# Optimization experiments

Measured on AMD Instinct MI355X. Metric: run time of the kernel, lower is better.

Reference implementation:

```python
import jax, jax.numpy as jnp
import numpy as np

NUM_HEADS = 16
WINDOW = 128
PERSIST = 16


def setup_inputs() -> dict:
    key = jax.random.key(0)
    ks = jax.random.split(key, 6)
    B, S, D, L = 2, 2048, 2048, 512
    sd = 1.0 / np.sqrt(D)
    sl = 1.0 / np.sqrt(L)
    return {
        "x": jax.random.normal(ks[0], (B, S, D), dtype=jnp.float32),
        "Wq": jax.random.normal(ks[1], (D, D), dtype=jnp.float32) * sd,
        "Wkv": jax.random.normal(ks[2], (D, L), dtype=jnp.float32) * sd,
        "Wk": jax.random.normal(ks[3], (L, D), dtype=jnp.float32) * sl,
        "Wv": jax.random.normal(ks[4], (L, D), dtype=jnp.float32) * sl,
        "Wo": jax.random.normal(ks[5], (D, D), dtype=jnp.float32) * sd,
    }


def reference(x, Wq, Wkv, Wk, Wv, Wo):
    B, S, D = x.shape
    H = NUM_HEADS
    hd = D // H
    scale = hd ** -0.5

    q = (x @ Wq).reshape(B, S, H, hd)
    kv_latent = x @ Wkv                      # MLA-style latent bottleneck
    k = (kv_latent @ Wk).reshape(B, S, H, hd)
    v = (kv_latent @ Wv).reshape(B, S, H, hd)

    # causal + sliding-window + persistent attention-sink mask
    qi = jnp.arange(S)[:, None]
    ki = jnp.arange(S)[None, :]
    mask = (ki <= qi) & ((qi - ki < WINDOW) | (ki < PERSIST))  # [S,S]

    scores = jnp.einsum("bqhd,bkhd->bhqk", q, k) * scale
    scores = jnp.where(mask[None, None], scores, jnp.finfo(scores.dtype).min)
    attn = jax.nn.softmax(scores, axis=-1)
    out = jnp.einsum("bhqk,bkhd->bqhd", attn, v).reshape(B, S, D)
    return out @ Wo
```

## Files before the change

kernel.cpp:

```cpp
#include <hip/hip_runtime.h>

typedef float f32x4 __attribute__((ext_vector_type(4)));
typedef float f32x16 __attribute__((ext_vector_type(16)));
typedef __bf16 bf16x8 __attribute__((ext_vector_type(8)));

__device__ __forceinline__ short f2bf(float f) {
    union { float f; unsigned u; } x; x.f = f;
    unsigned r = x.u + 0x7fffu + ((x.u >> 16) & 1u);
    return (short)(r >> 16);
}

__device__ __forceinline__ void store_out(float* p, float v) { *p = v; }
__device__ __forceinline__ void store_out(short* p, float v) { *p = f2bf(v); }

__device__ __forceinline__ void gload_lds16(const short* g, short* l) {
    __builtin_amdgcn_global_load_lds(
        (__attribute__((address_space(1))) void*)(void*)g,
        (__attribute__((address_space(3))) void*)l, 16, 0, 0);
}

__global__ void prep_all(const float* __restrict__ x, short* __restrict__ xb,
                         const float* __restrict__ Wq, const float* __restrict__ Wkv,
                         short* __restrict__ WqkvT) {
    __shared__ float tile[32][33];
    int id = blockIdx.x;
    const int t = threadIdx.x;
    if (id < 8192) {
        const int i = id * 256 + t;
        float4 v = ((const float4*)x)[i];
        ((short4*)xb)[i] = make_short4(f2bf(v.x), f2bf(v.y), f2bf(v.z), f2bf(v.w));
        return;
    }
    id -= 8192;
    const float* in; short* out; int R, C, xt, yt;
    if (id < 4096) { in = Wq;  out = WqkvT; R = 2048; C = 2048; xt = id & 63; yt = id >> 6; }
    else           { id -= 4096; in = Wkv; out = WqkvT + (size_t)2048 * 2048;
                     R = 2048; C = 512; xt = id & 15; yt = id >> 4; }
    const int c0 = xt * 32, r0 = yt * 32;
    const int tx = t & 31, ty = t >> 5;
#pragma unroll
    for (int i = 0; i < 32; i += 8)
        tile[ty + i][tx] = in[(size_t)(r0 + ty + i) * C + c0 + tx];
    __syncthreads();
#pragma unroll
    for (int i = 0; i < 32; i += 8)
        out[(size_t)(c0 + ty + i) * R + r0 + tx] = f2bf(tile[tx][ty + i]);
}

template <typename OutT>
__device__ __forceinline__ void gemm32_core(
    const short* __restrict__ A, const short* __restrict__ Bt, OutT* __restrict__ C,
    int m0, int n0, int K, int lda, int ldb, int ldc, short* sA, short* sB) {
    const int t = threadIdx.x;
    const int w = t >> 6, l = t & 63;
    const int wr = w >> 1, wc = w & 1;
    const int lrow = l & 31, lhalf = l >> 5;

    f32x16 acc[2][2] = {};

    const int r_off = w * 32 + (l >> 3);
    const int c8 = (((l & 7) ^ (l >> 3)) & 7) * 8;
    const short* aB = A + (size_t)(m0 + r_off) * lda + c8;
    const short* bB = Bt + (size_t)(n0 + r_off) * ldb + c8;
    short* sAw = sA + w * 2048;
    short* sBw = sB + w * 2048;

    for (int kk = 0; kk < K; kk += 64) {
#pragma unroll
        for (int p = 0; p < 4; ++p) {
            gload_lds16(aB + kk + (size_t)(p * 8) * lda, sAw + p * 512);
            gload_lds16(bB + kk + (size_t)(p * 8) * ldb, sBw + p * 512);
        }
        __syncthreads();
#pragma unroll
        for (int ks = 0; ks < 4; ++ks) {
            const int c = ks * 2 + lhalf;
            bf16x8 af[2], bfr[2];
#pragma unroll
            for (int mi = 0; mi < 2; ++mi) {
                const int m = wr * 64 + mi * 32 + lrow;
                af[mi] = *(const bf16x8*)&sA[m * 64 + (c ^ (m & 7)) * 8];
            }
#pragma unroll
            for (int ni = 0; ni < 2; ++ni) {
                const int n = wc * 64 + ni * 32 + lrow;
                bfr[ni] = *(const bf16x8*)&sB[n * 64 + (c ^ (n & 7)) * 8];
            }
#pragma unroll
            for (int mi = 0; mi < 2; ++mi)
#pragma unroll
                for (int ni = 0; ni < 2; ++ni)
                    acc[mi][ni] = __builtin_amdgcn_mfma_f32_32x32x16_bf16(
                        af[mi], bfr[ni], acc[mi][ni], 0, 0, 0);
        }
        __syncthreads();
    }
#pragma unroll
    for (int mi = 0; mi < 2; ++mi)
#pragma unroll
        for (int ni = 0; ni < 2; ++ni) {
            const int col = n0 + wc * 64 + ni * 32 + lrow;
#pragma unroll
            for (int r = 0; r < 16; ++r) {
                const int row = m0 + wr * 64 + mi * 32 + (r & 3) + 8 * (r >> 2) + 4 * lhalf;
                store_out(&C[(size_t)row * ldc + col], acc[mi][ni][r]);
            }
        }
}

__global__ __launch_bounds__(256, 2)
void gemm32qkv(const short* __restrict__ A, const short* __restrict__ Bt,
               short* __restrict__ C,
               const float* __restrict__ Wo, const float* __restrict__ Wk,
               const float* __restrict__ Wv,
               short* __restrict__ WoT, short* __restrict__ WkT,
               short* __restrict__ WvT) {
    __shared__ __align__(16) short sA[128 * 64];
    __shared__ __align__(16) short sB[128 * 64];
    int id = blockIdx.x;
    if (id < 640) {
        gemm32_core<short>(A, Bt, C, (id / 20) * 128, (id % 20) * 128,
                           2048, 2048, 2048, 2560, sA, sB);
        return;
    }
    id -= 640;
    float (*tile)[33] = (float(*)[33])sA;
    const float* in; short* out; int R, Cc, xt, yt;
    if (id < 4096)      { in = Wo; out = WoT; R = 2048; Cc = 2048; xt = id & 63; yt = id >> 6; }
    else if (id < 5120) { id -= 4096; in = Wk; out = WkT; R = 512; Cc = 2048; xt = id & 63; yt = id >> 6; }
    else                { id -= 5120; in = Wv; out = WvT; R = 512; Cc = 2048; xt = id & 63; yt = id >> 6; }
    const int c0 = xt * 32, r0 = yt * 32;
    const int t = threadIdx.x;
    const int tx = t & 31, ty = t >> 5;
#pragma unroll
    for (int i = 0; i < 32; i += 8)
        tile[ty + i][tx] = in[(size_t)(r0 + ty + i) * Cc + c0 + tx];
    __syncthreads();
#pragma unroll
    for (int i = 0; i < 32; i += 8)
        out[(size_t)(c0 + ty + i) * R + r0 + tx] = f2bf(tile[tx][ty + i]);
}

#define LBASE(buf, kh, ab) ((((((buf) << 1) | (kh)) << 1) | (ab)) * 8192)

#define STAGE(P, ld, tt, kh, buf, ab)                                   \
    do {                                                                \
        const int kb_ = (tt) * 64 + (kh) * 32;                          \
        const short* s_ = (P) + kb_;                                    \
        short* d_ = lds + LBASE(buf, kh, ab) + w * 512;                 \
        gload_lds16(s_, d_);                                            \
        gload_lds16(s_ + (size_t)128 * (ld), d_ + 4096);                \
    } while (0)

#define VM6 asm volatile("s_waitcnt vmcnt(6)" ::: "memory")

#define MFMA16(a, b, c) __builtin_amdgcn_mfma_f32_16x16x32_bf16(a, b, c, 0, 0, 0)

#define MM_ROW(mi, areg)                                                \
    acc[mi][0] = MFMA16(areg, bv0, acc[mi][0]);                         \
    acc[mi][1] = MFMA16(areg, bv1, acc[mi][1]);                         \
    acc[mi][2] = MFMA16(areg, bv2, acc[mi][2]);                         \
    acc[mi][3] = MFMA16(areg, bv3, acc[mi][3]);

#define HALFK(buf, kh, STG0, W0, STG1)                                  \
    {                                                                   \
        bf16x8 bv0, bv1, bv2, bv3;                                      \
        {                                                               \
            const short* Ab_ = lds + LBASE(buf, kh, 0) + (wm * 128) * 32 + foff; \
            const short* Bb_ = lds + LBASE(buf, kh, 1) + (wn * 64) * 32 + foff;  \
            bf16x8 a0_ = *(const bf16x8*)&Ab_[0];                       \
            bf16x8 a1_ = *(const bf16x8*)&Ab_[512];                     \
            bf16x8 a2_ = *(const bf16x8*)&Ab_[1024];                    \
            bf16x8 a3_ = *(const bf16x8*)&Ab_[1536];                    \
            bv0 = *(const bf16x8*)&Bb_[0];                              \
            bv1 = *(const bf16x8*)&Bb_[512];                            \
            bv2 = *(const bf16x8*)&Bb_[1024];                           \
            bv3 = *(const bf16x8*)&Bb_[1536];                           \
            STG0;                                                       \
            W0;                                                         \
            __builtin_amdgcn_s_barrier();                               \
            asm volatile("s_waitcnt lgkmcnt(0)" ::: "memory");          \
            __builtin_amdgcn_sched_barrier(0);                          \
            __builtin_amdgcn_s_setprio(1);                              \
            MM_ROW(0, a0_) MM_ROW(1, a1_) MM_ROW(2, a2_) MM_ROW(3, a3_) \
            __builtin_amdgcn_s_setprio(0);                              \
            __builtin_amdgcn_s_barrier();                               \
        }                                                               \
        {                                                               \
            const short* Ab_ = lds + LBASE(buf, kh, 0) + (wm * 128 + 64) * 32 + foff; \
            bf16x8 a0_ = *(const bf16x8*)&Ab_[0];                       \
            bf16x8 a1_ = *(const bf16x8*)&Ab_[512];                     \
            bf16x8 a2_ = *(const bf16x8*)&Ab_[1024];                    \
            bf16x8 a3_ = *(const bf16x8*)&Ab_[1536];                    \
            STG1;                                                       \
            __builtin_amdgcn_s_barrier();                               \
            asm volatile("s_waitcnt lgkmcnt(0)" ::: "memory");          \
            __builtin_amdgcn_sched_barrier(0);                          \
            __builtin_amdgcn_s_setprio(1);                              \
            MM_ROW(4, a0_) MM_ROW(5, a1_) MM_ROW(6, a2_) MM_ROW(7, a3_) \
            __builtin_amdgcn_s_setprio(0);                              \
            __builtin_amdgcn_s_barrier();                               \
        }                                                               \
    }

template <typename OutT>
__device__ __forceinline__ void gemm256_core(
    const short* __restrict__ A, const short* __restrict__ Bt, OutT* __restrict__ C,
    int m0, int n0, int K, int lda, int ldb, int ldc, short* lds) {
    const int t = threadIdx.x;
    const int w = t >> 6, l = t & 63;
    const int wm = w >> 2, wn = w & 3;
    const int l15 = l & 15, lc = l >> 4;

    const int su = (l & 7) ^ ((l >> 3) & 7);
    const int srow = (w << 4) + ((l >> 3) << 1) + (su >> 2);
    const int scol = (su & 3) << 3;
    const short* Ag = A + (size_t)(m0 + srow) * lda + scol;
    const short* Bg = Bt + (size_t)(n0 + srow) * ldb + scol;

    const int i3 = ((((l15 & 1) << 2) | lc) ^ ((l15 >> 1) & 7));
    const int foff = (l15 >> 1) * 64 + i3 * 8;

    f32x4 acc[8][4] = {};

    const int ntm1 = (K >> 6) - 1;
    const int niter = K >> 7;

    STAGE(Ag, lda, 0, 0, 0, 0);
    STAGE(Bg, ldb, 0, 0, 0, 1);
    STAGE(Ag, lda, 0, 1, 0, 0);
    STAGE(Bg, ldb, 0, 1, 0, 1);
    STAGE(Ag, lda, 1, 0, 1, 0);
    STAGE(Bg, ldb, 1, 0, 1, 1);
    asm volatile("s_waitcnt vmcnt(8)" ::: "memory");
    __builtin_amdgcn_s_barrier();

#pragma unroll 1
    for (int it = 0; it < niter; ++it) {
        const int tt = it * 2;
        const int t1 = tt + 1;
        const int t2 = (tt + 2 > ntm1) ? ntm1 : tt + 2;
        const int t3 = (tt + 3 > ntm1) ? ntm1 : tt + 3;
        HALFK(0, 0, STAGE(Ag, lda, t1, 1, 1, 0), VM6, STAGE(Bg, ldb, t1, 1, 1, 1))
        HALFK(0, 1, STAGE(Ag, lda, t2, 0, 0, 0), VM6, STAGE(Bg, ldb, t2, 0, 0, 1))
        HALFK(1, 0, STAGE(Ag, lda, t2, 1, 0, 0), VM6, STAGE(Bg, ldb, t2, 1, 0, 1))
        HALFK(1, 1, STAGE(Ag, lda, t3, 0, 1, 0), VM6, STAGE(Bg, ldb, t3, 0, 1, 1))
    }

    asm volatile("s_waitcnt vmcnt(0)" ::: "memory");

    const int crow = m0 + wm * 128 + lc * 4;
    const int ccol = n0 + wn * 64 + l15;
#pragma unroll
    for (int mi = 0; mi < 8; ++mi)
#pragma unroll
        for (int ni = 0; ni < 4; ++ni) {
            OutT* cp = C + (size_t)(crow + mi * 16) * ldc + ccol + ni * 16;
#pragma unroll
            for (int rr = 0; rr < 4; ++rr)
                store_out(cp + (size_t)rr * ldc, acc[mi][ni][rr]);
        }
}

__global__ __launch_bounds__(512, 2)
void gemm256_kv(const short* __restrict__ kvl, const short* __restrict__ WkT,
                short* __restrict__ kk, const short* __restrict__ WvT,
                short* __restrict__ vT) {
    extern __shared__ short lds[];
    int id = blockIdx.x;
    if (id < 128) {
        gemm256_core<short>(kvl, WkT, kk, (id >> 3) * 256, (id & 7) * 256,
                            512, 2560, 512, 2048, lds);
    } else {
        id -= 128;
        gemm256_core<short>(WvT, kvl, vT, (id >> 4) * 256, (id & 15) * 256,
                            512, 512, 2560, 4096, lds);
    }
}

#define LB2(s) ((s) * 12288)

#define STG2(ps, pt)                                                    \
    do {                                                                \
        const int kb_ = (pt) * 32;                                      \
        gload_lds16(Ag + kb_, lds + LB2(ps) + w * 512);                 \
        gload_lds16(Ag + kb_ + (size_t)128 * lda, lds + LB2(ps) + 4096 + w * 512); \
        gload_lds16(Bg + kb_, lds + LB2(ps) + 8192 + w * 512);          \
    } while (0)

#define PH2(s, ps, pt)                                                  \
    {                                                                   \
        const short* Ab_ = lds + LB2(s) + wm * 2048 + foff;             \
        const short* Bb_ = lds + LB2(s) + 8192 + wn * 2048 + foff;      \
        bf16x8 a0_ = *(const bf16x8*)&Ab_[0];                           \
        bf16x8 a1_ = *(const bf16x8*)&Ab_[512];                         \
        bf16x8 a2_ = *(const bf16x8*)&Ab_[1024];                        \
        bf16x8 a3_ = *(const bf16x8*)&Ab_[1536];                        \
        bf16x8 b0_ = *(const bf16x8*)&Bb_[0];                           \
        bf16x8 b1_ = *(const bf16x8*)&Bb_[512];                         \
        bf16x8 b2_ = *(const bf16x8*)&Bb_[1024];                        \
        bf16x8 b3_ = *(const bf16x8*)&Bb_[1536];                        \
        STG2(ps, pt);                                                   \
        asm volatile("s_waitcnt vmcnt(6)" ::: "memory");                \
        __builtin_amdgcn_s_barrier();                                   \
        asm volatile("s_waitcnt lgkmcnt(0)" ::: "memory");              \
        __builtin_amdgcn_sched_barrier(0);                              \
        __builtin_amdgcn_s_setprio(1);                                  \
        acc[0][0]=MFMA16(a0_,b0_,acc[0][0]); acc[0][1]=MFMA16(a0_,b1_,acc[0][1]); \
        acc[0][2]=MFMA16(a0_,b2_,acc[0][2]); acc[0][3]=MFMA16(a0_,b3_,acc[0][3]); \
        acc[1][0]=MFMA16(a1_,b0_,acc[1][0]); acc[1][1]=MFMA16(a1_,b1_,acc[1][1]); \
        acc[1][2]=MFMA16(a1_,b2_,acc[1][2]); acc[1][3]=MFMA16(a1_,b3_,acc[1][3]); \
        acc[2][0]=MFMA16(a2_,b0_,acc[2][0]); acc[2][1]=MFMA16(a2_,b1_,acc[2][1]); \
        acc[2][2]=MFMA16(a2_,b2_,acc[2][2]); acc[2][3]=MFMA16(a2_,b3_,acc[2][3]); \
        acc[3][0]=MFMA16(a3_,b0_,acc[3][0]); acc[3][1]=MFMA16(a3_,b1_,acc[3][1]); \
        acc[3][2]=MFMA16(a3_,b2_,acc[3][2]); acc[3][3]=MFMA16(a3_,b3_,acc[3][3]); \
        __builtin_amdgcn_s_setprio(0);                                  \
        __builtin_amdgcn_s_barrier();                                   \
    }

__global__ __launch_bounds__(512, 2)
void gemm_out(const short* __restrict__ A, const short* __restrict__ Bt,
              float* __restrict__ C, int K, int lda, int ldb, int ldc) {
    extern __shared__ short lds[];
    const int m0 = blockIdx.y * 256, n0 = blockIdx.x * 128;
    const int t = threadIdx.x;
    const int w = t >> 6, l = t & 63;
    const int wm = w >> 1, wn = w & 1;
    const int l15 = l & 15, lc = l >> 4;

    const int su = (l & 7) ^ ((l >> 3) & 7);
    const int srow = (w << 4) + ((l >> 3) << 1) + (su >> 2);
    const int scol = (su & 3) << 3;
    const short* Ag = A + (size_t)(m0 + srow) * lda + scol;
    const short* Bg = Bt + (size_t)(n0 + srow) * ldb + scol;

    const int i3 = ((((l15 & 1) << 2) | lc) ^ ((l15 >> 1) & 7));
    const int foff = (l15 >> 1) * 64 + i3 * 8;

    f32x4 acc[4][4] = {};

    const int nkh1 = (K >> 5) - 1;

    STG2(0, 0);
    STG2(1, 1);
    STG2(2, 2);
    asm volatile("s_waitcnt vmcnt(6)" ::: "memory");
    __builtin_amdgcn_s_barrier();

#pragma unroll 1
    for (int it = 0; it < (K >> 7); ++it) {
        const int h0 = it * 4;
        const int p3 = h0 + 3;
        const int p4 = (h0 + 4 > nkh1) ? nkh1 : h0 + 4;
        const int p5 = (h0 + 5 > nkh1) ? nkh1 : h0 + 5;
        const int p6 = (h0 + 6 > nkh1) ? nkh1 : h0 + 6;
        PH2(0, 3, p3)
        PH2(1, 0, p4)
        PH2(2, 1, p5)
        PH2(3, 2, p6)
    }

    asm volatile("s_waitcnt vmcnt(0)" ::: "memory");

    const int crow = m0 + wm * 64 + lc * 4;
    const int ccol = n0 + wn * 64 + l15;
#pragma unroll
    for (int mi = 0; mi < 4; ++mi)
#pragma unroll
        for (int ni = 0; ni < 4; ++ni) {
            float* cp = C + (size_t)(crow + mi * 16) * ldc + ccol + ni * 16;
#pragma unroll
            for (int rr = 0; rr < 4; ++rr)
                store_out(cp + (size_t)rr * ldc, acc[mi][ni][rr]);
        }
}

#define A_S 2048
#define A_D 2048
#define A_M 4096
#define A_HD 128
__global__ __launch_bounds__(256)
void attn_win3(const short* __restrict__ Q, const short* __restrict__ K,
               const short* __restrict__ vT, short* __restrict__ O, int ldq) {
    const int qt = blockIdx.x, h = blockIdx.y, b = blockIdx.z;
    const int Qs = qt * 64;
    const int t = threadIdx.x, w = t >> 6, l = t & 63;
    const int qs = Qs + w * 16;
    const int lg = l >> 4, ln = l & 15;
    const float SCALE = 0.088388347648318447f;

    __shared__ __align__(16) short sK[2][512 * 8];
    __shared__ __align__(16) short sV[2][512 * 8];
    __shared__ __align__(16) short sP[4][16][40];

    const size_t bS = (size_t)b * A_S;
    const short* qrow = Q + (bS + qs + ln) * ldq + h * A_HD;
    bf16x8 qf[4];
#pragma unroll
    for (int ks = 0; ks < 4; ++ks)
        qf[ks] = *(const bf16x8*)(qrow + ks * 32 + lg * 8);

    f32x4 o[8] = {};
    float lsum[4] = {0.f, 0.f, 0.f, 0.f};

    int C_lo = (Qs - 127) >> 5; if (C_lo < 0) C_lo = 0;
    const int C_hi = (Qs + 63) >> 5;
    const bool sink = C_lo > 0;
    const int total = (C_hi - C_lo + 1) + (sink ? 1 : 0);

    const int key0 = t >> 4, dseg0s = (t & 15) ^ (key0 & 7);
    const int d0 = t >> 2, ksg0 = (t & 3) ^ ((d0 >> 1) & 3);
    const int key1 = (256 + t) >> 4, dseg1s = (t & 15) ^ (key1 & 7);
    const int d1 = (256 + t) >> 2, ksg1 = (t & 3) ^ ((d1 >> 1) & 3);
    const short* Kb = K + bS * A_D + h * A_HD;
    const short* Vb = vT + (size_t)h * A_HD * A_M + b * A_S;

#define ASTAGE(kb, buf)                                                         \
    do {                                                                        \
        gload_lds16(Kb + (size_t)((kb) + key0) * A_D + dseg0s * 8,              \
                    &sK[buf][(size_t)(w * 64) * 8]);                            \
        gload_lds16(Vb + (size_t)d0 * A_M + (kb) + ksg0 * 8,                    \
                    &sV[buf][(size_t)(w * 64) * 8]);                            \
        gload_lds16(Kb + (size_t)((kb) + key1) * A_D + dseg1s * 8,              \
                    &sK[buf][(size_t)(256 + w * 64) * 8]);                      \
        gload_lds16(Vb + (size_t)d1 * A_M + (kb) + ksg1 * 8,                    \
                    &sV[buf][(size_t)(256 + w * 64) * 8]);                      \
    } while (0)

#define CHUNK_KB(ci) ((((sink) && (ci) == 0) ? 0 : (C_lo + (ci) - (sink ? 1 : 0))) * 32)

    ASTAGE(CHUNK_KB(0), 0);
    __syncthreads();

    for (int ci = 0; ci < total; ++ci) {
        if (ci + 1 < total) {
            const int nkb = CHUNK_KB(ci + 1);
            ASTAGE(nkb, (ci + 1) & 1);
        }
        const int kb = CHUNK_KB(ci);
        const int buf = ci & 1;
        const bool any = (kb < 16) || ((kb + 31 >= qs - 127) && (kb <= qs + 15));
        if (any) {
            f32x4 s0 = {0.f, 0.f, 0.f, 0.f}, s1 = {0.f, 0.f, 0.f, 0.f};
#pragma unroll
            for (int ks = 0; ks < 4; ++ks) {
                const int dsg = ks * 4 + lg;
                bf16x8 k0 = *(const bf16x8*)&sK[buf][(ln * 16 + (dsg ^ (ln & 7))) * 8];
                bf16x8 k1 = *(const bf16x8*)&sK[buf][((16 + ln) * 16 + (dsg ^ (ln & 7))) * 8];
                s0 = __builtin_amdgcn_mfma_f32_16x16x32_bf16(qf[ks], k0, s0, 0, 0, 0);
                s1 = __builtin_amdgcn_mfma_f32_16x16x32_bf16(qf[ks], k1, s1, 0, 0, 0);
            }
            const int k0i = kb + ln, k1i = kb + 16 + ln;
#pragma unroll
            for (int r = 0; r < 4; ++r) {
                const int qi = qs + lg * 4 + r;
                const bool m0 = (k0i <= qi) && ((qi - k0i < 128) || (k0i < 16));
                const bool m1 = (k1i <= qi) && ((qi - k1i < 128) || (k1i < 16));
                const float p0 = m0 ? __expf(s0[r] * SCALE) : 0.f;
                const float p1 = m1 ? __expf(s1[r] * SCALE) : 0.f;
                lsum[r] += p0 + p1;
                sP[w][lg * 4 + r][ln] = f2bf(p0);
                sP[w][lg * 4 + r][16 + ln] = f2bf(p1);
            }
            bf16x8 pf = *(const bf16x8*)&sP[w][ln][lg * 8];
#pragma unroll
            for (int dgi = 0; dgi < 8; ++dgi) {
                const int d = dgi * 16 + ln;
                bf16x8 vf = *(const bf16x8*)&sV[buf][(d * 4 + (lg ^ ((ln >> 1) & 3))) * 8];
                o[dgi] = __builtin_amdgcn_mfma_f32_16x16x32_bf16(pf, vf, o[dgi], 0, 0, 0);
            }
        }
        __syncthreads();
    }
#undef ASTAGE
#undef CHUNK_KB

#pragma unroll
    for (int r = 0; r < 4; ++r) {
        float s = lsum[r];
        s += __shfl_xor(s, 1); s += __shfl_xor(s, 2);
        s += __shfl_xor(s, 4); s += __shfl_xor(s, 8);
        const float inv = 1.0f / s;
        short* orow = O + (bS + qs + lg * 4 + r) * A_D + h * A_HD + ln;
#pragma unroll
        for (int dgi = 0; dgi < 8; ++dgi)
            orow[dgi * 16] = f2bf(o[dgi][r] * inv);
    }
}

extern "C" void kernel_launch(void* const* d_in, const int* in_sizes, int n_in,
                              void* d_out, int out_size, void* d_ws, size_t ws_size,
                              hipStream_t stream) {
    (void)in_sizes; (void)n_in; (void)out_size; (void)ws_size;
    const float* x   = (const float*)d_in[0];
    const float* Wq  = (const float*)d_in[1];
    const float* Wkv = (const float*)d_in[2];
    const float* Wk  = (const float*)d_in[3];
    const float* Wv  = (const float*)d_in[4];
    const float* Wo  = (const float*)d_in[5];
    float* out = (float*)d_out;

    const int B = 2, S = 2048, D = 2048, L = 512, H = 16;
    const int M = B * S;
    const int NQ = D + L;

    short* p = (short*)d_ws;
    short* xb    = p; p += (size_t)M * D;
    short* WqkvT = p; p += (size_t)NQ * D;
    short* WkT   = p; p += (size_t)D * L;
    short* WvT   = p; p += (size_t)D * L;
    short* WoT   = p; p += (size_t)D * D;
    short* qkv   = p; p += (size_t)M * NQ;
    short* kk    = p; p += (size_t)M * D;
    short* vT    = p; p += (size_t)D * M;
    short* ao    = p; p += (size_t)M * D;

    static bool attr_done = false;
    if (!attr_done) {
        hipFuncSetAttribute((const void*)&gemm256_kv,
                            hipFuncAttributeMaxDynamicSharedMemorySize, 131072);
        hipFuncSetAttribute((const void*)&gemm_out,
                            hipFuncAttributeMaxDynamicSharedMemorySize, 98304);
        attr_done = true;
    }

    prep_all<<<13312, 256, 0, stream>>>(x, xb, Wq, Wkv, WqkvT);
    gemm32qkv<<<6784, 256, 0, stream>>>(xb, WqkvT, qkv, Wo, Wk, Wv,
                                        WoT, WkT, WvT);
    gemm256_kv<<<256, 512, 131072, stream>>>(qkv + D, WkT, kk, WvT, vT);

    attn_win3<<<dim3(S / 64, H, B), 256, 0, stream>>>(qkv, kk, vT, ao, NQ);

    gemm_out<<<dim3(D / 128, M / 256), 512, 98304, stream>>>(
        ao, WoT, out, D, D, D, D);
}
```

Before: 260.6 us.

## Deepen gemm_out LDS pipeline from 4 to 6 stages

```diff
diff --git a/kernel.cpp b/kernel.cpp
--- a/kernel.cpp
+++ b/kernel.cpp
@@ -278,20 +278,20 @@
     }
 }
 
-#define LB2(s) ((s) * 12288)
-
-#define STG2(ps, pt)                                                    \
+#define LB6(s) ((s) * 12288)
+
+#define STG6(ps, pt)                                                    \
     do {                                                                \
         const int kb_ = (pt) * 32;                                      \
-        gload_lds16(Ag + kb_, lds + LB2(ps) + w * 512);                 \
-        gload_lds16(Ag + kb_ + (size_t)128 * lda, lds + LB2(ps) + 4096 + w * 512); \
-        gload_lds16(Bg + kb_, lds + LB2(ps) + 8192 + w * 512);          \
+        gload_lds16(Ag + kb_, lds + LB6(ps) + w * 512);                 \
+        gload_lds16(Ag + kb_ + (size_t)128 * lda, lds + LB6(ps) + 4096 + w * 512); \
+        gload_lds16(Bg + kb_, lds + LB6(ps) + 8192 + w * 512);          \
     } while (0)
 
-#define PH2(s, ps, pt)                                                  \
+#define PH6(s, ps, pt)                                                  \
     {                                                                   \
-        const short* Ab_ = lds + LB2(s) + wm * 2048 + foff;             \
-        const short* Bb_ = lds + LB2(s) + 8192 + wn * 2048 + foff;      \
+        const short* Ab_ = lds + LB6(s) + wm * 2048 + foff;             \
+        const short* Bb_ = lds + LB6(s) + 8192 + wn * 2048 + foff;      \
         bf16x8 a0_ = *(const bf16x8*)&Ab_[0];                           \
         bf16x8 a1_ = *(const bf16x8*)&Ab_[512];                         \
         bf16x8 a2_ = *(const bf16x8*)&Ab_[1024];                        \
@@ -300,8 +300,8 @@
         bf16x8 b1_ = *(const bf16x8*)&Bb_[512];                         \
         bf16x8 b2_ = *(const bf16x8*)&Bb_[1024];                        \
         bf16x8 b3_ = *(const bf16x8*)&Bb_[1536];                        \
-        STG2(ps, pt);                                                   \
-        asm volatile("s_waitcnt vmcnt(6)" ::: "memory");                \
+        STG6(ps, pt);                                                   \
+        asm volatile("s_waitcnt vmcnt(12)" ::: "memory");               \
         __builtin_amdgcn_s_barrier();                                   \
         asm volatile("s_waitcnt lgkmcnt(0)" ::: "memory");              \
         __builtin_amdgcn_sched_barrier(0);                              \
@@ -318,7 +318,7 @@
         __builtin_amdgcn_s_barrier();                                   \
     }
 
-__global__ __launch_bounds__(512, 2)
+__global__ __launch_bounds__(512, 1)
 void gemm_out(const short* __restrict__ A, const short* __restrict__ Bt,
               float* __restrict__ C, int K, int lda, int ldb, int ldc) {
     extern __shared__ short lds[];
@@ -339,26 +339,36 @@
 
     f32x4 acc[4][4] = {};
 
-    const int nkh1 = (K >> 5) - 1;
-
-    STG2(0, 0);
-    STG2(1, 1);
-    STG2(2, 2);
-    asm volatile("s_waitcnt vmcnt(6)" ::: "memory");
+    const int last = (K >> 5) - 1;
+
+    STG6(0, 0);
+    STG6(1, 1);
+    STG6(2, 2);
+    STG6(3, 3);
+    STG6(4, 4);
+    asm volatile("s_waitcnt vmcnt(12)" ::: "memory");
     __builtin_amdgcn_s_barrier();
 
 #pragma unroll 1
-    for (int it = 0; it < (K >> 7); ++it) {
-        const int h0 = it * 4;
-        const int p3 = h0 + 3;
-        const int p4 = (h0 + 4 > nkh1) ? nkh1 : h0 + 4;
-        const int p5 = (h0 + 5 > nkh1) ? nkh1 : h0 + 5;
-        const int p6 = (h0 + 6 > nkh1) ? nkh1 : h0 + 6;
-        PH2(0, 3, p3)
-        PH2(1, 0, p4)
-        PH2(2, 1, p5)
-        PH2(3, 2, p6)
-    }
+    for (int it = 0; it < ((K >> 5) - 4) / 6; ++it) {
+        const int p0 = it * 6;
+        const int q5  = (p0 + 5  > last) ? last : p0 + 5;
+        const int q6  = (p0 + 6  > last) ? last : p0 + 6;
+        const int q7  = (p0 + 7  > last) ? last : p0 + 7;
+        const int q8  = (p0 + 8  > last) ? last : p0 + 8;
+        const int q9  = (p0 + 9  > last) ? last : p0 + 9;
+        const int q10 = (p0 + 10 > last) ? last : p0 + 10;
+        PH6(0, 5, q5)
+        PH6(1, 0, q6)
+        PH6(2, 1, q7)
+        PH6(3, 2, q8)
+        PH6(4, 3, q9)
+        PH6(5, 4, q10)
+    }
+    PH6(0, 5, last)
+    PH6(1, 0, last)
+    PH6(2, 1, last)
+    PH6(3, 2, last)
 
     asm volatile("s_waitcnt vmcnt(0)" ::: "memory");
 
@@ -520,7 +530,7 @@
         hipFuncSetAttribute((const void*)&gemm256_kv,
                             hipFuncAttributeMaxDynamicSharedMemorySize, 131072);
         hipFuncSetAttribute((const void*)&gemm_out,
-                            hipFuncAttributeMaxDynamicSharedMemorySize, 98304);
+                            hipFuncAttributeMaxDynamicSharedMemorySize, 147456);
         attr_done = true;
     }
 
@@ -531,6 +541,6 @@
 
     attn_win3<<<dim3(S / 64, H, B), 256, 0, stream>>>(qkv, kk, vT, ao, NQ);
 
-    gemm_out<<<dim3(D / 128, M / 256), 512, 98304, stream>>>(
+    gemm_out<<<dim3(D / 128, M / 256), 512, 147456, stream>>>(
         ao, WoT, out, D, D, D, D);
 }
```

Result: no change. 263.0 us (+0.9%).
